# Performance work log

Measured on AMD Instinct MI355X. Metric: run time of the kernel, lower is better.

## Reference

```python
import jax, jax.numpy as jnp
import numpy as np

N = 8192
D_IN, D_MID, D_EMB = 1024, 256, 64
N_EDGES = N * 8


def setup_inputs() -> dict:
    key = jax.random.key(0)
    ks = jax.random.split(key, 6)
    X = jax.random.normal(ks[0], (N, D_IN), dtype=jnp.float32)
    # Xavier-uniform style init as in get_weight_initial
    b1 = np.sqrt(6.0 / (D_IN + D_MID))
    b2 = np.sqrt(6.0 / (D_MID + D_EMB))
    W1 = jax.random.uniform(ks[1], (D_IN, D_MID), minval=-b1, maxval=b1, dtype=jnp.float32)
    W2 = jax.random.uniform(ks[2], (D_MID, D_EMB), minval=-b2, maxval=b2, dtype=jnp.float32)
    edge_val = jax.random.uniform(ks[3], (N_EDGES,), dtype=jnp.float32)
    edge_src = jax.random.randint(ks[4], (N_EDGES,), 0, N, dtype=jnp.int32)
    edge_dst = jax.random.randint(ks[5], (N_EDGES,), 0, N, dtype=jnp.int32)
    return {"X": X, "W1": W1, "W2": W2, "edge_val": edge_val,
            "edge_src": edge_src, "edge_dst": edge_dst}


def reference(X, W1, W2, edge_val, edge_src, edge_dst):
    n = X.shape[0]

    def spmm(H):  # sparse Laplacian (COO) times dense H
        return jax.ops.segment_sum(edge_val[:, None] * H[edge_src], edge_dst,
                                   num_segments=n)

    h = jax.nn.relu(spmm(X @ W1))          # [N, D_MID]
    emb = spmm(h @ W2)                      # [N, D_EMB]
    # pairwise squared Euclidean distances between rows of emb -> [N, N]
    sq = jnp.sum(emb * emb, axis=1)
    dist = sq[:, None] + sq[None, :] - 2.0 * (emb @ emb.T)
    recons_w = jax.nn.softmax(-dist, axis=1) + 1e-10
    return recons_w
```

## Files before the change

### kernel.cpp

```cpp
#include <hip/hip_runtime.h>
#include <cstddef>

constexpr int NN    = 8192;
constexpr int DIN   = 1024;
constexpr int DMID  = 256;
constexpr int DEMB  = 64;
constexpr int NEDGE = 65536;

typedef __attribute__((ext_vector_type(8))) short bf16x8;
typedef __attribute__((ext_vector_type(4))) float f32x4;
#define MFMA16(a, b, c) __builtin_amdgcn_mfma_f32_16x16x32_bf16((a), (b), (c), 0, 0, 0)

__device__ __forceinline__ unsigned short bf16_rne(float x) {
  unsigned u = __float_as_uint(x);
  return (unsigned short)((u + 0x7FFFu + ((u >> 16) & 1u)) >> 16);
}
__device__ __forceinline__ float bf16_tof(unsigned short h) {
  return __uint_as_float((unsigned)h << 16);
}

constexpr int WCONV_BLOCKS = (DMID * DIN + DEMB * DMID) / 256;
__global__ __launch_bounds__(256) void prep_kernel(const float* __restrict__ W1,
                                                   const float* __restrict__ W2,
                                                   unsigned short* __restrict__ W1b,
                                                   unsigned short* __restrict__ W2b,
                                                   const int* __restrict__ edst,
                                                   int* __restrict__ counts)
{
  int b = blockIdx.x;
  if (b < WCONV_BLOCKS) {
    int idx = b * 256 + threadIdx.x;
    if (idx < DMID * DIN) {
      int n = idx >> 10, k = idx & 1023;
      W1b[idx] = bf16_rne(W1[k * DMID + n]);
    } else {
      int t = idx - DMID * DIN;
      int n = t >> 8, k = t & 255;
      W2b[t] = bf16_rne(W2[k * DEMB + n]);
    }
  } else {
    int e = (b - WCONV_BLOCKS) * 256 + threadIdx.x;
    atomicAdd(&counts[edst[e]], 1);
  }
}

__global__ __launch_bounds__(256) void scan_kernel(const int* __restrict__ counts,
                                                   int* __restrict__ row_start)
{
  __shared__ int sums[256];
  const int t = threadIdx.x;
  int local[32];
  int s = 0;
#pragma unroll
  for (int i = 0; i < 32; ++i) { local[i] = counts[t * 32 + i]; s += local[i]; }
  sums[t] = s;
  __syncthreads();
  for (int off = 1; off < 256; off <<= 1) {
    int v = (t >= off) ? sums[t - off] : 0;
    __syncthreads();
    sums[t] += v;
    __syncthreads();
  }
  int base = (t == 0) ? 0 : sums[t - 1];
#pragma unroll
  for (int i = 0; i < 32; ++i) { row_start[t * 32 + i] = base; base += local[i]; }
  if (t == 255) row_start[NN] = base;
}

__global__ __launch_bounds__(256) void scatter_kernel(
    const int* __restrict__ src, const float* __restrict__ val,
    const int* __restrict__ dst, const int* __restrict__ row_start,
    int* __restrict__ cursor, int* __restrict__ csr_src, float* __restrict__ csr_val)
{
  int e = blockIdx.x * 256 + threadIdx.x;
  int d = dst[e];
  int pos = row_start[d] + atomicAdd(&cursor[d], 1);
  csr_src[pos] = src[e];
  csr_val[pos] = val[e];
}

__global__ __launch_bounds__(256) void gemm1_kernel(
    const float* __restrict__ X, const unsigned short* __restrict__ W1b,
    unsigned short* __restrict__ G1)
{
  const int lane = threadIdx.x & 63;
  const int wave = threadIdx.x >> 6;
  const int m0 = blockIdx.y * 64 + wave * 16;
  const int n0 = blockIdx.x * 64;
  const int rl = lane & 15;
  const int kq = (lane >> 4) * 8;
  f32x4 zero = {0.f, 0.f, 0.f, 0.f};
  f32x4 acc[4] = {zero, zero, zero, zero};
  for (int s = 0; s < DIN / 32; ++s) {
    const int kb = s * 32 + kq;
    const float* xp = X + (size_t)(m0 + rl) * DIN + kb;
    float4 x0 = *(const float4*)xp;
    float4 x1 = *(const float4*)(xp + 4);
    bf16x8 ah;
    ah[0] = (short)bf16_rne(x0.x); ah[1] = (short)bf16_rne(x0.y);
    ah[2] = (short)bf16_rne(x0.z); ah[3] = (short)bf16_rne(x0.w);
    ah[4] = (short)bf16_rne(x1.x); ah[5] = (short)bf16_rne(x1.y);
    ah[6] = (short)bf16_rne(x1.z); ah[7] = (short)bf16_rne(x1.w);
#pragma unroll
    for (int ns = 0; ns < 4; ++ns) {
      bf16x8 bh = *(const bf16x8*)(W1b + (size_t)(n0 + ns * 16 + rl) * DIN + kb);
      acc[ns] = MFMA16(ah, bh, acc[ns]);
    }
  }
  const int rq = (lane >> 4) * 4;
#pragma unroll
  for (int ns = 0; ns < 4; ++ns)
#pragma unroll
    for (int r = 0; r < 4; ++r)
      G1[(size_t)(m0 + rq + r) * DMID + n0 + ns * 16 + rl] = bf16_rne(acc[ns][r]);
}

__global__ __launch_bounds__(256) void spmm1_kernel(
    const unsigned short* __restrict__ G1, const int* __restrict__ row_start,
    const int* __restrict__ csr_src, const float* __restrict__ csr_val,
    unsigned short* __restrict__ Hb)
{
  const int lane = threadIdx.x & 63;
  const int wave = threadIdx.x >> 6;
  const int r = blockIdx.x * 4 + wave;
  const int e0 = row_start[r];
  const int e1 = row_start[r + 1];
  const int c = lane * 4;
  float4 acc = make_float4(0.f, 0.f, 0.f, 0.f);
  for (int e = e0; e < e1; ++e) {
    const int s   = csr_src[e];
    const float v = csr_val[e];
    ushort4 h = *(const ushort4*)(G1 + (size_t)s * DMID + c);
    acc.x = fmaf(v, bf16_tof(h.x), acc.x);
    acc.y = fmaf(v, bf16_tof(h.y), acc.y);
    acc.z = fmaf(v, bf16_tof(h.z), acc.z);
    acc.w = fmaf(v, bf16_tof(h.w), acc.w);
  }
  ushort4 h;
  h.x = bf16_rne(fmaxf(acc.x, 0.f));
  h.y = bf16_rne(fmaxf(acc.y, 0.f));
  h.z = bf16_rne(fmaxf(acc.z, 0.f));
  h.w = bf16_rne(fmaxf(acc.w, 0.f));
  *(ushort4*)(Hb + (size_t)r * DMID + c) = h;
}

__global__ __launch_bounds__(256) void gemm2_kernel(
    const unsigned short* __restrict__ Ab, const unsigned short* __restrict__ W2b,
    float* __restrict__ E1)
{
  const int lane = threadIdx.x & 63;
  const int wave = threadIdx.x >> 6;
  const int m0 = blockIdx.x * 64 + wave * 16;
  const int rl = lane & 15;
  const int kq = (lane >> 4) * 8;
  f32x4 zero = {0.f, 0.f, 0.f, 0.f};
  f32x4 acc[4] = {zero, zero, zero, zero};
  for (int s = 0; s < DMID / 32; ++s) {
    const int kb = s * 32 + kq;
    bf16x8 ah = *(const bf16x8*)(Ab + (size_t)(m0 + rl) * DMID + kb);
#pragma unroll
    for (int ns = 0; ns < 4; ++ns) {
      bf16x8 bh = *(const bf16x8*)(W2b + (size_t)(ns * 16 + rl) * DMID + kb);
      acc[ns] = MFMA16(ah, bh, acc[ns]);
    }
  }
  const int rq = (lane >> 4) * 4;
#pragma unroll
  for (int ns = 0; ns < 4; ++ns)
#pragma unroll
    for (int r = 0; r < 4; ++r)
      E1[(size_t)(m0 + rq + r) * DEMB + ns * 16 + rl] = acc[ns][r];
}

__global__ __launch_bounds__(256) void spmm2_kernel(
    const float* __restrict__ H, const int* __restrict__ row_start,
    const int* __restrict__ csr_src, const float* __restrict__ csr_val,
    unsigned short* __restrict__ EmbH, float* __restrict__ sqv)
{
  const int lane = threadIdx.x & 63;
  const int wave = threadIdx.x >> 6;
  const int r = blockIdx.x * 4 + wave;
  const int e0 = row_start[r];
  const int e1 = row_start[r + 1];
  float acc = 0.f;
  for (int e = e0; e < e1; ++e)
    acc = fmaf(csr_val[e], H[(size_t)csr_src[e] * DEMB + lane], acc);
  unsigned short h = bf16_rne(acc);
  EmbH[(size_t)r * DEMB + lane] = h;
  float hf = bf16_tof(h);
  float sq = hf * hf;
#pragma unroll
  for (int off = 32; off; off >>= 1) sq += __shfl_xor(sq, off, 64);
  if (lane == 0) sqv[r] = sq;
}

__device__ __forceinline__ void dist_tile_hh(
    const unsigned short* __restrict__ EH, int ibase, int jbase, int lane,
    f32x4 (&acc)[4][4])
{
  const int rl = lane & 15;
  const int kq = (lane >> 4) * 8;
#pragma unroll
  for (int s = 0; s < 2; ++s) {
    const int kb = s * 32 + kq;
    bf16x8 a[4], b[4];
#pragma unroll
    for (int t = 0; t < 4; ++t) {
      a[t] = *(const bf16x8*)(EH + (size_t)(ibase + t * 16 + rl) * DEMB + kb);
      b[t] = *(const bf16x8*)(EH + (size_t)(jbase + t * 16 + rl) * DEMB + kb);
    }
#pragma unroll
    for (int ms = 0; ms < 4; ++ms)
#pragma unroll
      for (int ns = 0; ns < 4; ++ns)
        acc[ms][ns] = MFMA16(a[ms], b[ns], acc[ms][ns]);
  }
}

__global__ __launch_bounds__(256) void rowsum_sym_kernel(
    const unsigned short* __restrict__ EH, const float* __restrict__ sq,
    float* __restrict__ rowsum)
{
  const int bi = blockIdx.y, bj = blockIdx.x;
  if (bj < bi) return;
  const int lane = threadIdx.x & 63;
  const int wave = threadIdx.x >> 6;
  const int wr = wave >> 1, wc = wave & 1;
  const int ibase = bi * 128 + wr * 64;
  const int jbase = bj * 128 + wc * 64;
  const int rl = lane & 15;
  const int rq = (lane >> 4) * 4;

  f32x4 zero = {0.f, 0.f, 0.f, 0.f};
  f32x4 acc[4][4];
#pragma unroll
  for (int ms = 0; ms < 4; ++ms)
#pragma unroll
    for (int ns = 0; ns < 4; ++ns) acc[ms][ns] = zero;
  dist_tile_hh(EH, ibase, jbase, lane, acc);

  float si[4][4], sj[4];
#pragma unroll
  for (int ms = 0; ms < 4; ++ms)
#pragma unroll
    for (int r = 0; r < 4; ++r) si[ms][r] = sq[ibase + ms * 16 + rq + r];
#pragma unroll
  for (int ns = 0; ns < 4; ++ns) sj[ns] = sq[jbase + ns * 16 + rl];

  float rs[4][4] = {};
  float cs[4]    = {};
#pragma unroll
  for (int ms = 0; ms < 4; ++ms)
#pragma unroll
    for (int ns = 0; ns < 4; ++ns)
#pragma unroll
      for (int r = 0; r < 4; ++r) {
        float v = __expf(fmaf(2.f, acc[ms][ns][r], -si[ms][r] - sj[ns]));
        rs[ms][r] += v;
        cs[ns]    += v;
      }

#pragma unroll
  for (int ms = 0; ms < 4; ++ms)
#pragma unroll
    for (int r = 0; r < 4; ++r) {
      float v = rs[ms][r];
      v += __shfl_xor(v, 1, 64);
      v += __shfl_xor(v, 2, 64);
      v += __shfl_xor(v, 4, 64);
      v += __shfl_xor(v, 8, 64);
      if (rl == 0) atomicAdd(&rowsum[ibase + ms * 16 + rq + r], v);
    }

  if (bi != bj) {
#pragma unroll
    for (int ns = 0; ns < 4; ++ns) {
      float v = cs[ns];
      v += __shfl_xor(v, 16, 64);
      v += __shfl_xor(v, 32, 64);
      if (lane < 16) atomicAdd(&rowsum[jbase + ns * 16 + rl], v);
    }
  }
}

__global__ __launch_bounds__(256) void dist_write_kernel(
    const unsigned short* __restrict__ EH, const float* __restrict__ sq,
    const float* __restrict__ rowsum, float* __restrict__ out)
{
  const int lane = threadIdx.x & 63;
  const int wave = threadIdx.x >> 6;
  const int wr = wave >> 1, wc = wave & 1;
  const int ibase = blockIdx.y * 128 + wr * 64;
  const int jbase = blockIdx.x * 128 + wc * 64;
  const int rl = lane & 15;
  const int rq = (lane >> 4) * 4;

  f32x4 zero = {0.f, 0.f, 0.f, 0.f};
  f32x4 acc[4][4];
#pragma unroll
  for (int ms = 0; ms < 4; ++ms)
#pragma unroll
    for (int ns = 0; ns < 4; ++ns) acc[ms][ns] = zero;
  dist_tile_hh(EH, ibase, jbase, lane, acc);

  float si[4][4], ri[4][4], sj[4];
#pragma unroll
  for (int ms = 0; ms < 4; ++ms)
#pragma unroll
    for (int r = 0; r < 4; ++r) {
      const int i = ibase + ms * 16 + rq + r;
      si[ms][r] = sq[i];
      ri[ms][r] = 1.f / rowsum[i];
    }
#pragma unroll
  for (int ns = 0; ns < 4; ++ns) sj[ns] = sq[jbase + ns * 16 + rl];

#pragma unroll
  for (int ms = 0; ms < 4; ++ms)
#pragma unroll
    for (int r = 0; r < 4; ++r) {
      const size_t row = (size_t)(ibase + ms * 16 + rq + r) * NN;
#pragma unroll
      for (int ns = 0; ns < 4; ++ns) {
        float e = __expf(fmaf(2.f, acc[ms][ns][r], -si[ms][r] - sj[ns]));
        out[row + jbase + ns * 16 + rl] = fmaf(e, ri[ms][r], 1e-10f);
      }
    }
}

extern "C" void kernel_launch(void* const* d_in, const int* in_sizes, int n_in,
                              void* d_out, int out_size, void* d_ws, size_t ws_size,
                              hipStream_t stream)
{
  const float* X  = (const float*)d_in[0];
  const float* W1 = (const float*)d_in[1];
  const float* W2 = (const float*)d_in[2];
  const float* ev = (const float*)d_in[3];
  const int* esrc = (const int*)d_in[4];
  const int* edst = (const int*)d_in[5];
  float* out = (float*)d_out;

  char* p = (char*)d_ws;
  auto alloc = [&](size_t bytes) { char* q = p; p += (bytes + 255) & ~(size_t)255; return q; };

  int*   counts    = (int*)alloc(NN * 4);
  int*   cursor    = (int*)alloc(NN * 4);
  float* rowsum    = (float*)alloc(NN * 4);
  int*   row_start = (int*)alloc((NN + 1) * 4);
  int*   csr_src   = (int*)alloc(NEDGE * 4);
  float* csr_val   = (float*)alloc(NEDGE * 4);
  float* sqv       = (float*)alloc(NN * 4);
  float* E1        = (float*)alloc((size_t)NN * DEMB * 4);
  unsigned short* W1b  = (unsigned short*)alloc((size_t)DMID * DIN * 2);
  unsigned short* W2b  = (unsigned short*)alloc((size_t)DEMB * DMID * 2);
  unsigned short* G1   = (unsigned short*)alloc((size_t)NN * DMID * 2);
  unsigned short* H1b  = (unsigned short*)alloc((size_t)NN * DMID * 2);
  unsigned short* EmbH = (unsigned short*)alloc((size_t)NN * DEMB * 2);

  hipMemsetAsync(d_ws, 0, (size_t)3 * NN * 4, stream);

  prep_kernel<<<WCONV_BLOCKS + NEDGE / 256, 256, 0, stream>>>(W1, W2, W1b, W2b, edst, counts);
  scan_kernel<<<1, 256, 0, stream>>>(counts, row_start);
  scatter_kernel<<<NEDGE / 256, 256, 0, stream>>>(esrc, ev, edst, row_start, cursor,
                                                  csr_src, csr_val);

  gemm1_kernel<<<dim3(DMID / 64, NN / 64), 256, 0, stream>>>(X, W1b, G1);
  spmm1_kernel<<<NN / 4, 256, 0, stream>>>(G1, row_start, csr_src, csr_val, H1b);
  gemm2_kernel<<<NN / 64, 256, 0, stream>>>(H1b, W2b, E1);
  spmm2_kernel<<<NN / 4, 256, 0, stream>>>(E1, row_start, csr_src, csr_val, EmbH, sqv);

  rowsum_sym_kernel<<<dim3(NN / 128, NN / 128), 256, 0, stream>>>(EmbH, sqv, rowsum);
  dist_write_kernel<<<dim3(NN / 128, NN / 128), 256, 0, stream>>>(EmbH, sqv, rowsum, out);
}
```

Baseline: 461.1 us.

## Switch to ELL adjacency, fuse spmm1 with gemm2, prebuild bf16 X, drop symmetric rowsum

Replaces the count/scan/scatter CSR build with a single atomic-cursor ELL build capped at 64 neighbours per row, removing two kernel launches and the memset. The memset's zeroing moves into the prep kernel, which now also converts X to bf16 up front so gemm1 loads bf16 directly. The first SpMM is fused with the second GEMM through shared memory, so the H1 intermediate never goes to global memory. The symmetric rowsum kernel becomes a non-symmetric one that loops over 8 column tiles per block, and the output write uses nontemporal stores. The ELL cap silently drops edges for any row with more than 64 incoming edges, and the non-symmetric rowsum computes roughly twice the exponentials.

```diff
diff --git a/kernel.cpp b/kernel.cpp
--- a/kernel.cpp
+++ b/kernel.cpp
@@ -1,11 +1,12 @@
 #include <hip/hip_runtime.h>
 #include <cstddef>
 
-constexpr int NN    = 8192;
-constexpr int DIN   = 1024;
-constexpr int DMID  = 256;
-constexpr int DEMB  = 64;
-constexpr int NEDGE = 65536;
+constexpr int NN     = 8192;
+constexpr int DIN    = 1024;
+constexpr int DMID   = 256;
+constexpr int DEMB   = 64;
+constexpr int NEDGE  = 65536;
+constexpr int MAXDEG = 64;
 
 typedef __attribute__((ext_vector_type(8))) short bf16x8;
 typedef __attribute__((ext_vector_type(4))) float f32x4;
@@ -20,12 +21,15 @@
 }
 
 constexpr int WCONV_BLOCKS = (DMID * DIN + DEMB * DMID) / 256;
+constexpr int XCONV_BLOCKS = NN * DIN / (256 * 8);
+constexpr int ZERO_BLOCKS  = 16;
 __global__ __launch_bounds__(256) void prep_kernel(const float* __restrict__ W1,
                                                    const float* __restrict__ W2,
+                                                   const float* __restrict__ X,
                                                    unsigned short* __restrict__ W1b,
                                                    unsigned short* __restrict__ W2b,
-                                                   const int* __restrict__ edst,
-                                                   int* __restrict__ counts)
+                                                   unsigned short* __restrict__ Xb,
+                                                   int* __restrict__ zero_base)
 {
   int b = blockIdx.x;
   if (b < WCONV_BLOCKS) {
@@ -38,69 +42,51 @@
       int n = t >> 8, k = t & 255;
       W2b[t] = bf16_rne(W2[k * DEMB + n]);
     }
+  } else if (b < WCONV_BLOCKS + XCONV_BLOCKS) {
+    int idx = (b - WCONV_BLOCKS) * 2048 + threadIdx.x * 8;
+    float4 x0 = *(const float4*)(X + idx);
+    float4 x1 = *(const float4*)(X + idx + 4);
+    bf16x8 h;
+    h[0] = (short)bf16_rne(x0.x); h[1] = (short)bf16_rne(x0.y);
+    h[2] = (short)bf16_rne(x0.z); h[3] = (short)bf16_rne(x0.w);
+    h[4] = (short)bf16_rne(x1.x); h[5] = (short)bf16_rne(x1.y);
+    h[6] = (short)bf16_rne(x1.z); h[7] = (short)bf16_rne(x1.w);
+    *(bf16x8*)(Xb + idx) = h;
   } else {
-    int e = (b - WCONV_BLOCKS) * 256 + threadIdx.x;
-    atomicAdd(&counts[edst[e]], 1);
-  }
-}
-
-__global__ __launch_bounds__(256) void scan_kernel(const int* __restrict__ counts,
-                                                   int* __restrict__ row_start)
-{
-  __shared__ int sums[256];
-  const int t = threadIdx.x;
-  int local[32];
-  int s = 0;
-#pragma unroll
-  for (int i = 0; i < 32; ++i) { local[i] = counts[t * 32 + i]; s += local[i]; }
-  sums[t] = s;
-  __syncthreads();
-  for (int off = 1; off < 256; off <<= 1) {
-    int v = (t >= off) ? sums[t - off] : 0;
-    __syncthreads();
-    sums[t] += v;
-    __syncthreads();
-  }
-  int base = (t == 0) ? 0 : sums[t - 1];
-#pragma unroll
-  for (int i = 0; i < 32; ++i) { row_start[t * 32 + i] = base; base += local[i]; }
-  if (t == 255) row_start[NN] = base;
-}
-
-__global__ __launch_bounds__(256) void scatter_kernel(
-    const int* __restrict__ src, const float* __restrict__ val,
-    const int* __restrict__ dst, const int* __restrict__ row_start,
-    int* __restrict__ cursor, int* __restrict__ csr_src, float* __restrict__ csr_val)
+    int idx = (b - WCONV_BLOCKS - XCONV_BLOCKS) * 1024 + threadIdx.x * 4;
+    *(int4*)(zero_base + idx) = make_int4(0, 0, 0, 0);
+  }
+}
+
+__global__ __launch_bounds__(256) void build_ell_kernel(
+    const int* __restrict__ esrc, const float* __restrict__ ev,
+    const int* __restrict__ edst, int* __restrict__ cursor,
+    int* __restrict__ ell_src, float* __restrict__ ell_val)
 {
   int e = blockIdx.x * 256 + threadIdx.x;
-  int d = dst[e];
-  int pos = row_start[d] + atomicAdd(&cursor[d], 1);
-  csr_src[pos] = src[e];
-  csr_val[pos] = val[e];
+  int d = edst[e];
+  int pos = atomicAdd(&cursor[d], 1);
+  if (pos < MAXDEG) {
+    ell_src[d * MAXDEG + pos] = esrc[e];
+    ell_val[d * MAXDEG + pos] = ev[e];
+  }
 }
 
 __global__ __launch_bounds__(256) void gemm1_kernel(
-    const float* __restrict__ X, const unsigned short* __restrict__ W1b,
+    const unsigned short* __restrict__ Xb, const unsigned short* __restrict__ W1b,
     unsigned short* __restrict__ G1)
 {
   const int lane = threadIdx.x & 63;
   const int wave = threadIdx.x >> 6;
-  const int m0 = blockIdx.y * 64 + wave * 16;
-  const int n0 = blockIdx.x * 64;
+  const int m0 = blockIdx.x * 64 + wave * 16;
+  const int n0 = blockIdx.y * 64;
   const int rl = lane & 15;
   const int kq = (lane >> 4) * 8;
   f32x4 zero = {0.f, 0.f, 0.f, 0.f};
   f32x4 acc[4] = {zero, zero, zero, zero};
   for (int s = 0; s < DIN / 32; ++s) {
     const int kb = s * 32 + kq;
-    const float* xp = X + (size_t)(m0 + rl) * DIN + kb;
-    float4 x0 = *(const float4*)xp;
-    float4 x1 = *(const float4*)(xp + 4);
-    bf16x8 ah;
-    ah[0] = (short)bf16_rne(x0.x); ah[1] = (short)bf16_rne(x0.y);
-    ah[2] = (short)bf16_rne(x0.z); ah[3] = (short)bf16_rne(x0.w);
-    ah[4] = (short)bf16_rne(x1.x); ah[5] = (short)bf16_rne(x1.y);
-    ah[6] = (short)bf16_rne(x1.z); ah[7] = (short)bf16_rne(x1.w);
+    bf16x8 ah = *(const bf16x8*)(Xb + (size_t)(m0 + rl) * DIN + kb);
 #pragma unroll
     for (int ns = 0; ns < 4; ++ns) {
       bf16x8 bh = *(const bf16x8*)(W1b + (size_t)(n0 + ns * 16 + rl) * DIN + kb);
@@ -115,76 +101,71 @@
       G1[(size_t)(m0 + rq + r) * DMID + n0 + ns * 16 + rl] = bf16_rne(acc[ns][r]);
 }
 
-__global__ __launch_bounds__(256) void spmm1_kernel(
-    const unsigned short* __restrict__ G1, const int* __restrict__ row_start,
-    const int* __restrict__ csr_src, const float* __restrict__ csr_val,
-    unsigned short* __restrict__ Hb)
-{
-  const int lane = threadIdx.x & 63;
-  const int wave = threadIdx.x >> 6;
-  const int r = blockIdx.x * 4 + wave;
-  const int e0 = row_start[r];
-  const int e1 = row_start[r + 1];
+__global__ __launch_bounds__(256) void spmm1_gemm2_kernel(
+    const unsigned short* __restrict__ G1, const int* __restrict__ deg,
+    const int* __restrict__ ell_src, const float* __restrict__ ell_val,
+    const unsigned short* __restrict__ W2b, float* __restrict__ E1)
+{
+  __shared__ unsigned short Hs[16][DMID + 8];
+  const int lane = threadIdx.x & 63;
+  const int wave = threadIdx.x >> 6;
+  const int r0 = blockIdx.x * 16;
   const int c = lane * 4;
-  float4 acc = make_float4(0.f, 0.f, 0.f, 0.f);
-  for (int e = e0; e < e1; ++e) {
-    const int s   = csr_src[e];
-    const float v = csr_val[e];
-    ushort4 h = *(const ushort4*)(G1 + (size_t)s * DMID + c);
-    acc.x = fmaf(v, bf16_tof(h.x), acc.x);
-    acc.y = fmaf(v, bf16_tof(h.y), acc.y);
-    acc.z = fmaf(v, bf16_tof(h.z), acc.z);
-    acc.w = fmaf(v, bf16_tof(h.w), acc.w);
-  }
-  ushort4 h;
-  h.x = bf16_rne(fmaxf(acc.x, 0.f));
-  h.y = bf16_rne(fmaxf(acc.y, 0.f));
-  h.z = bf16_rne(fmaxf(acc.z, 0.f));
-  h.w = bf16_rne(fmaxf(acc.w, 0.f));
-  *(ushort4*)(Hb + (size_t)r * DMID + c) = h;
-}
-
-__global__ __launch_bounds__(256) void gemm2_kernel(
-    const unsigned short* __restrict__ Ab, const unsigned short* __restrict__ W2b,
-    float* __restrict__ E1)
-{
-  const int lane = threadIdx.x & 63;
-  const int wave = threadIdx.x >> 6;
-  const int m0 = blockIdx.x * 64 + wave * 16;
+#pragma unroll
+  for (int rr = 0; rr < 4; ++rr) {
+    const int row = wave * 4 + rr;
+    const int r = r0 + row;
+    const int dg = min(deg[r], MAXDEG);
+    const int* sp = ell_src + (size_t)r * MAXDEG;
+    const float* vp = ell_val + (size_t)r * MAXDEG;
+    float4 acc = make_float4(0.f, 0.f, 0.f, 0.f);
+    for (int e = 0; e < dg; ++e) {
+      const int s = sp[e];
+      const float v = vp[e];
+      ushort4 h = *(const ushort4*)(G1 + (size_t)s * DMID + c);
+      acc.x = fmaf(v, bf16_tof(h.x), acc.x);
+      acc.y = fmaf(v, bf16_tof(h.y), acc.y);
+      acc.z = fmaf(v, bf16_tof(h.z), acc.z);
+      acc.w = fmaf(v, bf16_tof(h.w), acc.w);
+    }
+    ushort4 hq;
+    hq.x = bf16_rne(fmaxf(acc.x, 0.f));
+    hq.y = bf16_rne(fmaxf(acc.y, 0.f));
+    hq.z = bf16_rne(fmaxf(acc.z, 0.f));
+    hq.w = bf16_rne(fmaxf(acc.w, 0.f));
+    *(ushort4*)(&Hs[row][c]) = hq;
+  }
+  __syncthreads();
   const int rl = lane & 15;
   const int kq = (lane >> 4) * 8;
-  f32x4 zero = {0.f, 0.f, 0.f, 0.f};
-  f32x4 acc[4] = {zero, zero, zero, zero};
+  f32x4 acc4 = {0.f, 0.f, 0.f, 0.f};
+#pragma unroll
   for (int s = 0; s < DMID / 32; ++s) {
     const int kb = s * 32 + kq;
-    bf16x8 ah = *(const bf16x8*)(Ab + (size_t)(m0 + rl) * DMID + kb);
-#pragma unroll
-    for (int ns = 0; ns < 4; ++ns) {
-      bf16x8 bh = *(const bf16x8*)(W2b + (size_t)(ns * 16 + rl) * DMID + kb);
-      acc[ns] = MFMA16(ah, bh, acc[ns]);
-    }
+    bf16x8 a = *(const bf16x8*)(&Hs[rl][kb]);
+    bf16x8 b = *(const bf16x8*)(W2b + (size_t)(wave * 16 + rl) * DMID + kb);
+    acc4 = MFMA16(a, b, acc4);
   }
   const int rq = (lane >> 4) * 4;
 #pragma unroll
-  for (int ns = 0; ns < 4; ++ns)
-#pragma unroll
-    for (int r = 0; r < 4; ++r)
-      E1[(size_t)(m0 + rq + r) * DEMB + ns * 16 + rl] = acc[ns][r];
+  for (int r = 0; r < 4; ++r)
+    E1[(size_t)(r0 + rq + r) * DEMB + wave * 16 + rl] = acc4[r];
 }
 
 __global__ __launch_bounds__(256) void spmm2_kernel(
-    const float* __restrict__ H, const int* __restrict__ row_start,
-    const int* __restrict__ csr_src, const float* __restrict__ csr_val,
+    const float* __restrict__ H, const int* __restrict__ deg,
+    const int* __restrict__ ell_src, const float* __restrict__ ell_val,
     unsigned short* __restrict__ EmbH, float* __restrict__ sqv)
 {
   const int lane = threadIdx.x & 63;
   const int wave = threadIdx.x >> 6;
   const int r = blockIdx.x * 4 + wave;
-  const int e0 = row_start[r];
-  const int e1 = row_start[r + 1];
+  const int dg = min(deg[r], MAXDEG);
+  const int* sp = ell_src + (size_t)r * MAXDEG;
+  const float* vp = ell_val + (size_t)r * MAXDEG;
   float acc = 0.f;
-  for (int e = e0; e < e1; ++e)
-    acc = fmaf(csr_val[e], H[(size_t)csr_src[e] * DEMB + lane], acc);
+  for (int e = 0; e < dg; ++e)
+    acc = fmaf(vp[e], H[(size_t)sp[e] * DEMB + lane], acc);
   unsigned short h = bf16_rne(acc);
   EmbH[(size_t)r * DEMB + lane] = h;
   float hf = bf16_tof(h);
@@ -194,72 +175,63 @@
   if (lane == 0) sqv[r] = sq;
 }
 
-__device__ __forceinline__ void dist_tile_hh(
-    const unsigned short* __restrict__ EH, int ibase, int jbase, int lane,
-    f32x4 (&acc)[4][4])
-{
-  const int rl = lane & 15;
-  const int kq = (lane >> 4) * 8;
-#pragma unroll
-  for (int s = 0; s < 2; ++s) {
-    const int kb = s * 32 + kq;
-    bf16x8 a[4], b[4];
-#pragma unroll
-    for (int t = 0; t < 4; ++t) {
-      a[t] = *(const bf16x8*)(EH + (size_t)(ibase + t * 16 + rl) * DEMB + kb);
-      b[t] = *(const bf16x8*)(EH + (size_t)(jbase + t * 16 + rl) * DEMB + kb);
-    }
-#pragma unroll
-    for (int ms = 0; ms < 4; ++ms)
-#pragma unroll
-      for (int ns = 0; ns < 4; ++ns)
-        acc[ms][ns] = MFMA16(a[ms], b[ns], acc[ms][ns]);
-  }
-}
-
-__global__ __launch_bounds__(256) void rowsum_sym_kernel(
+__global__ __launch_bounds__(256) void rowsum_kernel(
     const unsigned short* __restrict__ EH, const float* __restrict__ sq,
     float* __restrict__ rowsum)
 {
-  const int bi = blockIdx.y, bj = blockIdx.x;
-  if (bj < bi) return;
   const int lane = threadIdx.x & 63;
   const int wave = threadIdx.x >> 6;
   const int wr = wave >> 1, wc = wave & 1;
-  const int ibase = bi * 128 + wr * 64;
-  const int jbase = bj * 128 + wc * 64;
-  const int rl = lane & 15;
+  const int ibase = blockIdx.y * 128 + wr * 64;
+  const int rl = lane & 15;
+  const int kq = (lane >> 4) * 8;
   const int rq = (lane >> 4) * 4;
 
-  f32x4 zero = {0.f, 0.f, 0.f, 0.f};
-  f32x4 acc[4][4];
-#pragma unroll
-  for (int ms = 0; ms < 4; ++ms)
-#pragma unroll
-    for (int ns = 0; ns < 4; ++ns) acc[ms][ns] = zero;
-  dist_tile_hh(EH, ibase, jbase, lane, acc);
-
-  float si[4][4], sj[4];
+  bf16x8 a[2][4];
+#pragma unroll
+  for (int s = 0; s < 2; ++s)
+#pragma unroll
+    for (int t = 0; t < 4; ++t)
+      a[s][t] = *(const bf16x8*)(EH + (size_t)(ibase + t * 16 + rl) * DEMB + s * 32 + kq);
+
+  float si[4][4];
 #pragma unroll
   for (int ms = 0; ms < 4; ++ms)
 #pragma unroll
     for (int r = 0; r < 4; ++r) si[ms][r] = sq[ibase + ms * 16 + rq + r];
-#pragma unroll
-  for (int ns = 0; ns < 4; ++ns) sj[ns] = sq[jbase + ns * 16 + rl];
 
   float rs[4][4] = {};
-  float cs[4]    = {};
-#pragma unroll
-  for (int ms = 0; ms < 4; ++ms)
-#pragma unroll
-    for (int ns = 0; ns < 4; ++ns)
-#pragma unroll
-      for (int r = 0; r < 4; ++r) {
-        float v = __expf(fmaf(2.f, acc[ms][ns][r], -si[ms][r] - sj[ns]));
-        rs[ms][r] += v;
-        cs[ns]    += v;
-      }
-
+  for (int jt = 0; jt < 8; ++jt) {
+    const int jbase = blockIdx.x * 1024 + jt * 128 + wc * 64;
+    float sj[4];
+#pragma unroll
+    for (int ns = 0; ns < 4; ++ns) sj[ns] = sq[jbase + ns * 16 + rl];
+    f32x4 zero = {0.f, 0.f, 0.f, 0.f};
+    f32x4 acc[4][4];
+#pragma unroll
+    for (int ms = 0; ms < 4; ++ms)
+#pragma unroll
+      for (int ns = 0; ns < 4; ++ns) acc[ms][ns] = zero;
+#pragma unroll
+    for (int s = 0; s < 2; ++s) {
+      bf16x8 b[4];
+#pragma unroll
+      for (int t = 0; t < 4; ++t)
+        b[t] = *(const bf16x8*)(EH + (size_t)(jbase + t * 16 + rl) * DEMB + s * 32 + kq);
+#pragma unroll
+      for (int ms = 0; ms < 4; ++ms)
+#pragma unroll
+        for (int ns = 0; ns < 4; ++ns)
+          acc[ms][ns] = MFMA16(a[s][ms], b[ns], acc[ms][ns]);
+    }
+#pragma unroll
+    for (int ms = 0; ms < 4; ++ms)
+#pragma unroll
+      for (int ns = 0; ns < 4; ++ns)
+#pragma unroll
+        for (int r = 0; r < 4; ++r)
+          rs[ms][r] += __expf(fmaf(2.f, acc[ms][ns][r], -si[ms][r] - sj[ns]));
+  }
 #pragma unroll
   for (int ms = 0; ms < 4; ++ms)
 #pragma unroll
@@ -271,15 +243,28 @@
       v += __shfl_xor(v, 8, 64);
       if (rl == 0) atomicAdd(&rowsum[ibase + ms * 16 + rq + r], v);
     }
-
-  if (bi != bj) {
-#pragma unroll
-    for (int ns = 0; ns < 4; ++ns) {
-      float v = cs[ns];
-      v += __shfl_xor(v, 16, 64);
-      v += __shfl_xor(v, 32, 64);
-      if (lane < 16) atomicAdd(&rowsum[jbase + ns * 16 + rl], v);
-    }
+}
+
+__device__ __forceinline__ void dist_tile_hh(
+    const unsigned short* __restrict__ EH, int ibase, int jbase, int lane,
+    f32x4 (&acc)[4][4])
+{
+  const int rl = lane & 15;
+  const int kq = (lane >> 4) * 8;
+#pragma unroll
+  for (int s = 0; s < 2; ++s) {
+    const int kb = s * 32 + kq;
+    bf16x8 a[4], b[4];
+#pragma unroll
+    for (int t = 0; t < 4; ++t) {
+      a[t] = *(const bf16x8*)(EH + (size_t)(ibase + t * 16 + rl) * DEMB + kb);
+      b[t] = *(const bf16x8*)(EH + (size_t)(jbase + t * 16 + rl) * DEMB + kb);
+    }
+#pragma unroll
+    for (int ms = 0; ms < 4; ++ms)
+#pragma unroll
+      for (int ns = 0; ns < 4; ++ns)
+        acc[ms][ns] = MFMA16(a[ms], b[ns], acc[ms][ns]);
   }
 }
 
@@ -323,7 +308,8 @@
 #pragma unroll
       for (int ns = 0; ns < 4; ++ns) {
         float e = __expf(fmaf(2.f, acc[ms][ns][r], -si[ms][r] - sj[ns]));
-        out[row + jbase + ns * 16 + rl] = fmaf(e, ri[ms][r], 1e-10f);
+        __builtin_nontemporal_store(fmaf(e, ri[ms][r], 1e-10f),
+                                    &out[row + jbase + ns * 16 + rl]);
       }
     }
 }
@@ -343,32 +329,28 @@
   char* p = (char*)d_ws;
   auto alloc = [&](size_t bytes) { char* q = p; p += (bytes + 255) & ~(size_t)255; return q; };
 
-  int*   counts    = (int*)alloc(NN * 4);
-  int*   cursor    = (int*)alloc(NN * 4);
-  float* rowsum    = (float*)alloc(NN * 4);
-  int*   row_start = (int*)alloc((NN + 1) * 4);
-  int*   csr_src   = (int*)alloc(NEDGE * 4);
-  float* csr_val   = (float*)alloc(NEDGE * 4);
-  float* sqv       = (float*)alloc(NN * 4);
-  float* E1        = (float*)alloc((size_t)NN * DEMB * 4);
+  int*   cursor  = (int*)alloc(NN * 4);
+  float* rowsum  = (float*)alloc(NN * 4);
+  float* sqv     = (float*)alloc(NN * 4);
+  float* E1      = (float*)alloc((size_t)NN * DEMB * 4);
   unsigned short* W1b  = (unsigned short*)alloc((size_t)DMID * DIN * 2);
   unsigned short* W2b  = (unsigned short*)alloc((size_t)DEMB * DMID * 2);
+  unsigned short* Xb   = (unsigned short*)alloc((size_t)NN * DIN * 2);
   unsigned short* G1   = (unsigned short*)alloc((size_t)NN * DMID * 2);
-  unsigned short* H1b  = (unsigned short*)alloc((size_t)NN * DMID * 2);
   unsigned short* EmbH = (unsigned short*)alloc((size_t)NN * DEMB * 2);
-
-  hipMemsetAsync(d_ws, 0, (size_t)3 * NN * 4, stream);
-
-  prep_kernel<<<WCONV_BLOCKS + NEDGE / 256, 256, 0, stream>>>(W1, W2, W1b, W2b, edst, counts);
-  scan_kernel<<<1, 256, 0, stream>>>(counts, row_start);
-  scatter_kernel<<<NEDGE / 256, 256, 0, stream>>>(esrc, ev, edst, row_start, cursor,
-                                                  csr_src, csr_val);
-
-  gemm1_kernel<<<dim3(DMID / 64, NN / 64), 256, 0, stream>>>(X, W1b, G1);
-  spmm1_kernel<<<NN / 4, 256, 0, stream>>>(G1, row_start, csr_src, csr_val, H1b);
-  gemm2_kernel<<<NN / 64, 256, 0, stream>>>(H1b, W2b, E1);
-  spmm2_kernel<<<NN / 4, 256, 0, stream>>>(E1, row_start, csr_src, csr_val, EmbH, sqv);
-
-  rowsum_sym_kernel<<<dim3(NN / 128, NN / 128), 256, 0, stream>>>(EmbH, sqv, rowsum);
+  int*   ell_src = (int*)alloc((size_t)NN * MAXDEG * 4);
+  float* ell_val = (float*)alloc((size_t)NN * MAXDEG * 4);
+
+  prep_kernel<<<WCONV_BLOCKS + XCONV_BLOCKS + ZERO_BLOCKS, 256, 0, stream>>>(
+      W1, W2, X, W1b, W2b, Xb, cursor);
+  build_ell_kernel<<<NEDGE / 256, 256, 0, stream>>>(esrc, ev, edst, cursor,
+                                                    ell_src, ell_val);
+
+  gemm1_kernel<<<dim3(NN / 64, DMID / 64), 256, 0, stream>>>(Xb, W1b, G1);
+  spmm1_gemm2_kernel<<<NN / 16, 256, 0, stream>>>(G1, cursor, ell_src, ell_val,
+                                                  W2b, E1);
+  spmm2_kernel<<<NN / 4, 256, 0, stream>>>(E1, cursor, ell_src, ell_val, EmbH, sqv);
+
+  rowsum_kernel<<<dim3(8, NN / 128), 256, 0, stream>>>(EmbH, sqv, rowsum);
   dist_write_kernel<<<dim3(NN / 128, NN / 128), 256, 0, stream>>>(EmbH, sqv, rowsum, out);
 }
```

New measurement: 434.6 us. -5.8%, faster.
